# Kernel tuning notes

Hardware: AMD Instinct MI355X
Metric: run time of the kernel (lower is better)

The kernel has to match this reference:

```python
import jax, jax.numpy as jnp
import numpy as np

OBS_LEN, PRED_LEN = 20, 30
H, EMB, MLP, NOISE, HEADS = 32, 16, 64, 8, 4
N, B, G = 131072, 4096, 32  # total agents, scenes, agents per scene
NEG = -1e9


def layernorm(x, g, b, eps=1e-5):
    m = x.mean(-1, keepdims=True)
    v = ((x - m) ** 2).mean(-1, keepdims=True)
    return (x - m) / jnp.sqrt(v + eps) * g + b


def setup_inputs():
    key = jax.random.key(0)
    ks = iter(jax.random.split(key, 40))
    rn = lambda shape, s=0.1: jax.random.normal(next(ks), shape, jnp.float32) * s
    starts = np.arange(B, dtype=np.int64) * G
    return {
        "obs_traj": rn((OBS_LEN, N, 2), 1.0),
        "obs_traj_rel": rn((OBS_LEN, N, 2), 1.0),
        "start_end_seq": jnp.stack([jnp.asarray(starts), jnp.asarray(starts + G)], 1).astype(jnp.int32),
        "noise_z": rn((NOISE,), 1.0),
        "enc_emb_w": rn((EMB, 2)), "enc_emb_b": rn((EMB,)),
        "enc_wih": rn((4 * H, EMB)), "enc_whh": rn((4 * H, H)),
        "enc_bih": rn((4 * H,)), "enc_bhh": rn((4 * H,)),
        "lne_g": jnp.ones((H,), jnp.float32), "lne_b": jnp.zeros((H,), jnp.float32),
        "wq": rn((H, H)), "wk": rn((H, H)), "wv": rn((H, H)), "wo": rn((H, H)),
        "lnc_g": jnp.ones((2 * H,), jnp.float32), "lnc_b": jnp.zeros((2 * H,), jnp.float32),
        "mlp1_w": rn((MLP, 2 * H)), "mlp1_b": rn((MLP,)),
        "mlp2_w": rn((H - NOISE, MLP)), "mlp2_b": rn((H - NOISE,)),
        "dec_emb_w": rn((EMB, 2)), "dec_emb_b": rn((EMB,)),
        "dec_wih": rn((4 * H, EMB)), "dec_whh": rn((4 * H, H)),
        "dec_bih": rn((4 * H,)), "dec_bhh": rn((4 * H,)),
        "dec_out_w": rn((2, H)), "dec_out_b": rn((2,)),
    }


def _forward(obs_traj, obs_traj_rel, noise_z,
             enc_emb_w, enc_emb_b, enc_wih, enc_whh, enc_bih, enc_bhh,
             lne_g, lne_b, wq, wk, wv, wo, lnc_g, lnc_b,
             mlp1_w, mlp1_b, mlp2_w, mlp2_b,
             dec_emb_w, dec_emb_b, dec_wih, dec_whh, dec_bih, dec_bhh,
             dec_out_w, dec_out_b, se_np):
    n = obs_traj_rel.shape[1]
    # ---- Encoder: linear spatial embedding + single-layer LSTM over obs window
    emb = obs_traj_rel @ enc_emb_w.T + enc_emb_b  # (T, n, EMB)

    def enc_step(carry, x):
        h, c = carry
        gates = x @ enc_wih.T + enc_bih + h @ enc_whh.T + enc_bhh
        i, f, g, o = jnp.split(gates, 4, -1)
        c = jax.nn.sigmoid(f) * c + jax.nn.sigmoid(i) * jnp.tanh(g)
        h = jax.nn.sigmoid(o) * jnp.tanh(c)
        return (h, c), None

    z0 = jnp.zeros((n, H), emb.dtype)
    (h_enc, _), _ = jax.lax.scan(enc_step, (z0, z0), emb)
    h_enc = layernorm(h_enc, lne_g, lne_b)  # (n, H)

    # ---- Ragged per-scene self-attention, padded to max scene size
    lengths = se_np[:, 1] - se_np[:, 0]
    L = int(lengths.max())
    pos = np.arange(L)
    mask = pos[None, :] < lengths[:, None]                # (B, L) valid slots
    idx = np.where(mask, se_np[:, :1] + pos[None, :], 0)  # (B, L)
    Hp = h_enc[jnp.asarray(idx)]                          # (B, L, H)
    b = mask.shape[0]
    dh = H // HEADS

    def heads(w):
        return (Hp @ w.T).reshape(b, L, HEADS, dh).transpose(0, 2, 1, 3)

    q, k, v = heads(wq), heads(wk), heads(wv)
    scores = jnp.einsum('bhqd,bhkd->bhqk', q, k) / jnp.sqrt(jnp.float32(dh))
    scores = jnp.where(jnp.asarray(mask)[:, None, None, :], scores, NEG)
    attn = jnp.einsum('bhqk,bhkd->bhqd', jax.nn.softmax(scores, -1), v)
    attn = attn.transpose(0, 2, 1, 3).reshape(b, L, H) @ wo.T  # (B, L, H)
    flat = jnp.asarray(np.where(mask, idx, n).reshape(-1))     # invalid -> pad row n
    attn_s = jnp.zeros((n + 1, H), attn.dtype).at[flat].set(attn.reshape(-1, H))[:n]

    # ---- Decoder context MLP (LeakyReLU after every Linear, incl. last) + noise
    ctx = layernorm(jnp.concatenate([h_enc, attn_s], -1), lnc_g, lnc_b)
    x = jax.nn.leaky_relu(ctx @ mlp1_w.T + mlp1_b)
    x = jax.nn.leaky_relu(x @ mlp2_w.T + mlp2_b)  # (n, H-NOISE)
    dec_h = jnp.concatenate([x, jnp.broadcast_to(noise_z, (n, NOISE))], -1)
    dec_c = jnp.zeros_like(dec_h)

    # ---- Temporal decoder: LSTM rollout of PRED_LEN relative displacements
    def dec_step(carry, _):
        h, c, last_rel = carry
        e = last_rel @ dec_emb_w.T + dec_emb_b
        gates = e @ dec_wih.T + dec_bih + h @ dec_whh.T + dec_bhh
        i, f, g, o = jnp.split(gates, 4, -1)
        c = jax.nn.sigmoid(f) * c + jax.nn.sigmoid(i) * jnp.tanh(g)
        h = jax.nn.sigmoid(o) * jnp.tanh(c)
        rel = h @ dec_out_w.T + dec_out_b
        return (h, c, rel), rel

    _, preds = jax.lax.scan(dec_step, (dec_h, dec_c, obs_traj_rel[-1]), None, length=PRED_LEN)
    return preds  # (PRED_LEN, n, 2)


def reference(obs_traj, obs_traj_rel, start_end_seq, noise_z,
              enc_emb_w, enc_emb_b, enc_wih, enc_whh, enc_bih, enc_bhh,
              lne_g, lne_b, wq, wk, wv, wo, lnc_g, lnc_b,
              mlp1_w, mlp1_b, mlp2_w, mlp2_b,
              dec_emb_w, dec_emb_b, dec_wih, dec_whh, dec_bih, dec_bhh,
              dec_out_w, dec_out_b):
    se_np = np.asarray(start_end_seq)
    return _forward(obs_traj, obs_traj_rel, noise_z,
                    enc_emb_w, enc_emb_b, enc_wih, enc_whh, enc_bih, enc_bhh,
                    lne_g, lne_b, wq, wk, wv, wo, lnc_g, lnc_b,
                    mlp1_w, mlp1_b, mlp2_w, mlp2_b,
                    dec_emb_w, dec_emb_b, dec_wih, dec_whh, dec_bih, dec_bhh,
                    dec_out_w, dec_out_b, se_np)
```

## Files before the change

kernel.cpp:

```cpp
#include <hip/hip_runtime.h>
#include <hip/hip_bf16.h>
#include <stdint.h>

typedef unsigned short u16;
typedef unsigned int   u32;

#define NTOT 131072

typedef __bf16 bf16x8 __attribute__((ext_vector_type(8)));
typedef float  f32x4  __attribute__((ext_vector_type(4)));

typedef bf16x8 bf16x8_a __attribute__((may_alias));
typedef int4   int4_a   __attribute__((may_alias));
typedef u16    u16_a    __attribute__((may_alias));
typedef u32    u32_a    __attribute__((may_alias));
typedef float  f32_a    __attribute__((may_alias));
typedef float4 float4_a __attribute__((may_alias));
typedef float2 float2_a __attribute__((may_alias));
typedef f32x4  f32x4_a  __attribute__((may_alias));

__device__ __forceinline__ void lds_fence(){
  asm volatile("s_waitcnt lgkmcnt(0)" ::: "memory");
}

__device__ __forceinline__ float b2f(u16 u){ return __uint_as_float(((u32)u)<<16); }
__device__ __forceinline__ u16 f2b(float f){
  u32 x = __float_as_uint(f);
  return (u16)((x + 0x7fffu + ((x>>16)&1u)) >> 16);
}
__device__ __forceinline__ u16 bfb(float f){
  union { __bf16 b; u16 u; } c; c.b = (__bf16)f; return c.u;
}
__device__ __forceinline__ u32 pk2(float a, float b){
  return (u32)bfb(a) | (((u32)bfb(b))<<16);
}
__device__ __forceinline__ float ld(const u16* p, long long i, bool f32m){
  return f32m ? ((const f32_a*)p)[i] : b2f(((const u16_a*)p)[i]);
}
__device__ __forceinline__ float2 ld2(const u16* p, long long i, bool f32m){
  if (f32m) return ((const float2_a*)(const void*)p)[i];
  u32 v = ((const u32_a*)p)[i];
  float2 r; r.x = b2f((u16)(v & 0xffffu)); r.y = b2f((u16)(v >> 16)); return r;
}
__device__ __forceinline__ bool is_f32(const u16* ones){
  return ((const u32_a*)ones)[0] == 0x3F800000u;
}

__device__ __forceinline__ void lstm_cell(float i_, float f_, float g_, float o_,
                                          float& c, float& h){
  float ai = __expf(-i_);
  float ef = __expf(-f_);
  float gc = fminf(fmaxf(g_, -40.f), 40.f);
  float tg = __expf(2.f*gc);
  float t1 = (1.f+ai)*(tg+1.f);
  float num = c*t1 + (tg-1.f)*(1.f+ef);
  c = num * __builtin_amdgcn_rcpf((1.f+ef)*t1);
  float ao = __expf(-o_);
  float tc = __expf(2.f*c);
  h = (tc-1.f) * __builtin_amdgcn_rcpf((1.f+ao)*(tc+1.f));
}

__device__ __forceinline__ bf16x8 mk_frag(const u16* W, int ldW, int n, int kbase, bool f32m){
  union { bf16x8 v; u16 s[8]; } u;
  if (f32m){
    const f32_a* p = (const f32_a*)W + (size_t)n*ldW + kbase;
    float4 x0 = *reinterpret_cast<const float4_a*>(p);
    float4 x1 = *reinterpret_cast<const float4_a*>(p+4);
    u.s[0]=f2b(x0.x); u.s[1]=f2b(x0.y); u.s[2]=f2b(x0.z); u.s[3]=f2b(x0.w);
    u.s[4]=f2b(x1.x); u.s[5]=f2b(x1.y); u.s[6]=f2b(x1.z); u.s[7]=f2b(x1.w);
  } else {
    #pragma unroll
    for (int j=0;j<8;++j) u.s[j] = ((const u16_a*)W)[(size_t)n*ldW + kbase + j];
  }
  return u.v;
}
__device__ __forceinline__ void split_hilo(const float* x, bf16x8& hi, bf16x8& lo){
  union { bf16x8 v; u16 s[8]; } uh, ul;
  #pragma unroll
  for (int j=0;j<8;++j){ u16 hb=f2b(x[j]); uh.s[j]=hb; ul.s[j]=f2b(x[j]-b2f(hb)); }
  hi=uh.v; lo=ul.v;
}

__global__ void prep_kernel(const u16* __restrict__ wih, const u16* __restrict__ whh,
                            const u16* __restrict__ bih, const u16* __restrict__ bhh,
                            const u16* __restrict__ dwih, const u16* __restrict__ dwhh,
                            const u16* __restrict__ dbih, const u16* __restrict__ dbhh,
                            const u16* __restrict__ dembw, const u16* __restrict__ dembb,
                            const u16* __restrict__ doutw, const u16* __restrict__ doutb,
                            const u16* __restrict__ lng,
                            u16* __restrict__ WTe, u16* __restrict__ WTd,
                            float* __restrict__ biasd, float* __restrict__ wemo)
{
  const bool f32m = is_f32(lng);
  int tid = blockIdx.x*blockDim.x + threadIdx.x;
  int nthr = gridDim.x*blockDim.x;
  for (int idx = tid; idx < 128*96; idx += nthr){
    int rw = idx/96, k = idx - rw*96;
    float ve;
    if (k < 64){
      int kc = k & 31; int q = kc >> 3, r = kc & 7;
      int u = (r < 4) ? (q*4 + r) : (16 + q*4 + (r-4));
      ve = ld(whh, rw*32+u, f32m);
    } else {
      int kk = k - 64; int q = kk >> 3, j = kk & 7;
      if (j < 4){
        ve = ld(wih, rw*16 + q*4+j, f32m);
      } else if (q == 0 && j == 4){
        ve = ld(bih, rw, f32m) + ld(bhh, rw, f32m);
      } else if (q == 0 && j == 5){
        float bse = ld(bih, rw, f32m) + ld(bhh, rw, f32m);
        ve = bse - b2f(f2b(bse));
      } else {
        ve = 0.f;
      }
    }
    WTe[idx] = f2b(ve);
    if (k < 64){
      int kc = k & 31; int q = kc >> 3, r = kc & 7;
      int u = (r < 4) ? (q*4 + r) : (16 + q*4 + (r-4));
      float wem0 = 0.f, wem1 = 0.f;
      #pragma unroll
      for (int j=0; j<16; ++j){
        float wv = ld(dwih, rw*16+j, f32m);
        wem0 += wv*ld(dembw, j*2,   f32m);
        wem1 += wv*ld(dembw, j*2+1, f32m);
      }
      float wp = ld(dwhh, rw*32+u, f32m)
               + wem0*ld(doutw, u,    f32m)
               + wem1*ld(doutw, 32+u, f32m);
      u16 hi = f2b(wp);
      WTd[rw*64 + k] = (k < 32) ? hi : f2b(wp - b2f(hi));
    }
  }
  if (tid < 128){
    int rw = tid;
    float wem0 = 0.f, wem1 = 0.f, wdb = 0.f;
    #pragma unroll
    for (int j=0; j<16; ++j){
      float wv = ld(dwih, rw*16+j, f32m);
      wem0 += wv*ld(dembw, j*2,   f32m);
      wem1 += wv*ld(dembw, j*2+1, f32m);
      wdb  += wv*ld(dembb, j,     f32m);
    }
    float bp = ld(dbih, rw, f32m) + ld(dbhh, rw, f32m) + wdb
             + wem0*ld(doutb, 0, f32m) + wem1*ld(doutb, 1, f32m);
    biasd[rw] = bp;
    wemo[rw*2]   = wem0;
    wemo[rw*2+1] = wem1;
  }
}

__global__ __launch_bounds__(256, 1) void enc_kernel(
    const u16* __restrict__ obs_rel, const u16* __restrict__ WT,
    const u16* __restrict__ embw, const u16* __restrict__ embb,
    const u16* __restrict__ lng, const u16* __restrict__ lnb,
    float* __restrict__ hln)
{
  const bool f32m = is_f32(lng);
  const int lane = threadIdx.x & 63;
  const int wvi  = threadIdx.x >> 6;
  const int col  = lane & 15;
  const int quad = lane >> 4;
  const int base = (blockIdx.x*4 + wvi)*16;

  bf16x8 wf[8][3];
  #pragma unroll
  for (int g=0; g<8; ++g)
    #pragma unroll
    for (int c=0; c<3; ++c)
      wf[g][c] = *reinterpret_cast<const bf16x8_a*>(WT + (g*16+col)*96 + c*32 + quad*8);

  float ew0[4], ew1[4], ebv[4];
  #pragma unroll
  for (int jj=0; jj<4; ++jj){
    int j = quad*4+jj;
    ew0[jj]=ld(embw, j*2, f32m); ew1[jj]=ld(embw, j*2+1, f32m); ebv[jj]=ld(embb, j, f32m);
  }
  const u32 onespk = (quad == 0) ? 0x3F803F80u : 0u;

  union FR { bf16x8 v; u32 w[4]; };
  FR x0, x1, x2;
  x0.w[0]=x0.w[1]=x0.w[2]=x0.w[3]=0;
  x1.w[0]=x1.w[1]=x1.w[2]=x1.w[3]=0;
  x2.w[2] = onespk; x2.w[3] = 0;

  float c0[4]={0,0,0,0}, c1[4]={0,0,0,0};
  float hA[4]={0,0,0,0}, hB[4]={0,0,0,0};

  float2 rv = ld2(obs_rel, (long long)(base + col), f32m);

  #pragma unroll 1
  for (int t=0; t<20; ++t){
    float2 rnx = rv;
    if (t < 19) rnx = ld2(obs_rel, (long long)(t+1)*NTOT + base + col, f32m);
    float e0 = ew0[0]*rv.x + ew1[0]*rv.y + ebv[0];
    float e1 = ew0[1]*rv.x + ew1[1]*rv.y + ebv[1];
    float e2 = ew0[2]*rv.x + ew1[2]*rv.y + ebv[2];
    float e3 = ew0[3]*rv.x + ew1[3]*rv.y + ebv[3];
    x2.w[0] = pk2(e0, e1);
    x2.w[1] = pk2(e2, e3);

    f32x4 acc[8];
    #pragma unroll
    for (int g=0; g<8; ++g){ f32x4 zz = {0.f,0.f,0.f,0.f};
      acc[g] = __builtin_amdgcn_mfma_f32_16x16x32_bf16(wf[g][0], x0.v, zz, 0,0,0); }
    #pragma unroll
    for (int g=0; g<8; ++g)
      acc[g] = __builtin_amdgcn_mfma_f32_16x16x32_bf16(wf[g][1], x1.v, acc[g], 0,0,0);
    #pragma unroll
    for (int g=0; g<8; ++g)
      acc[g] = __builtin_amdgcn_mfma_f32_16x16x32_bf16(wf[g][2], x2.v, acc[g], 0,0,0);

    #pragma unroll
    for (int reg=0; reg<4; ++reg){
      lstm_cell(acc[0][reg], acc[2][reg], acc[4][reg], acc[6][reg], c0[reg], hA[reg]);
      lstm_cell(acc[1][reg], acc[3][reg], acc[5][reg], acc[7][reg], c1[reg], hB[reg]);
    }
    u16 a0b=bfb(hA[0]), a1b=bfb(hA[1]), a2b=bfb(hA[2]), a3b=bfb(hA[3]);
    u16 b0b=bfb(hB[0]), b1b=bfb(hB[1]), b2b=bfb(hB[2]), b3b=bfb(hB[3]);
    x0.w[0] = (u32)a0b | ((u32)a1b<<16);
    x0.w[1] = (u32)a2b | ((u32)a3b<<16);
    x0.w[2] = (u32)b0b | ((u32)b1b<<16);
    x0.w[3] = (u32)b2b | ((u32)b3b<<16);
    x1.w[0] = pk2(hA[0]-b2f(a0b), hA[1]-b2f(a1b));
    x1.w[1] = pk2(hA[2]-b2f(a2b), hA[3]-b2f(a3b));
    x1.w[2] = pk2(hB[0]-b2f(b0b), hB[1]-b2f(b1b));
    x1.w[3] = pk2(hB[2]-b2f(b2b), hB[3]-b2f(b3b));
    rv = rnx;
  }

  float sm = 0.f, sq = 0.f;
  #pragma unroll
  for (int reg=0; reg<4; ++reg){
    sm += hA[reg]+hB[reg];
    sq += hA[reg]*hA[reg]+hB[reg]*hB[reg];
  }
  sm += __shfl_xor(sm, 16, 64); sm += __shfl_xor(sm, 32, 64);
  sq += __shfl_xor(sq, 16, 64); sq += __shfl_xor(sq, 32, 64);
  float mean = sm*(1.f/32.f);
  float var  = sq*(1.f/32.f) - mean*mean;
  float rstd = rsqrtf(fmaxf(var, 0.f) + 1e-5f);
  float4 yA, yB;
  {
    float gA0=ld(lng,quad*4+0,f32m), gA1=ld(lng,quad*4+1,f32m), gA2=ld(lng,quad*4+2,f32m), gA3=ld(lng,quad*4+3,f32m);
    float bA0=ld(lnb,quad*4+0,f32m), bA1=ld(lnb,quad*4+1,f32m), bA2=ld(lnb,quad*4+2,f32m), bA3=ld(lnb,quad*4+3,f32m);
    float gB0=ld(lng,16+quad*4+0,f32m), gB1=ld(lng,16+quad*4+1,f32m), gB2=ld(lng,16+quad*4+2,f32m), gB3=ld(lng,16+quad*4+3,f32m);
    float bB0=ld(lnb,16+quad*4+0,f32m), bB1=ld(lnb,16+quad*4+1,f32m), bB2=ld(lnb,16+quad*4+2,f32m), bB3=ld(lnb,16+quad*4+3,f32m);
    yA.x=(hA[0]-mean)*rstd*gA0+bA0; yA.y=(hA[1]-mean)*rstd*gA1+bA1;
    yA.z=(hA[2]-mean)*rstd*gA2+bA2; yA.w=(hA[3]-mean)*rstd*gA3+bA3;
    yB.x=(hB[0]-mean)*rstd*gB0+bB0; yB.y=(hB[1]-mean)*rstd*gB1+bB1;
    yB.z=(hB[2]-mean)*rstd*gB2+bB2; yB.w=(hB[3]-mean)*rstd*gB3+bB3;
  }
  size_t a = (size_t)(base + col);
  *reinterpret_cast<float4_a*>(hln + a*32 + quad*4)      = yA;
  *reinterpret_cast<float4_a*>(hln + a*32 + 16 + quad*4) = yB;
}

__global__ __launch_bounds__(256, 1) void mid_kernel(
    const int* __restrict__ se, const float* __restrict__ hln,
    const u16* __restrict__ wq, const u16* __restrict__ wk,
    const u16* __restrict__ wvp, const u16* __restrict__ wo,
    const u16* __restrict__ lncg, const u16* __restrict__ lncb,
    const u16* __restrict__ m1w, const u16* __restrict__ m1b,
    const u16* __restrict__ m2w, const u16* __restrict__ m2b,
    const u16* __restrict__ noise, float* __restrict__ dech0)
{
  __shared__ float hsL[2][32][36];
  __shared__ float kL [2][32][36];
  __shared__ float vL [2][32][36];
  __shared__ float qL [2][32][36];
  __shared__ float aoL[2][32][36];
  __shared__ float cxL[4][16][68];

  const bool f32m = is_f32(lncg);
  const int lane = threadIdx.x & 63;
  const int wvi  = threadIdx.x >> 6;
  const int col  = lane & 15;
  const int quad = lane >> 4;
  const int sc_l = wvi >> 1;
  const int half = wvi & 1;
  const int a_lo = half*16;
  const int scene = blockIdx.x*2 + sc_l;

  const int s0  = se[2*scene];
  int len = se[2*scene+1] - s0;
  if (len > 32) len = 32; if (len < 0) len = 0;

  {
    int ar = a_lo + (lane>>2);
    long long g = (long long)s0 + ar;
    if (g > NTOT-1) g = NTOT-1; if (g < 0) g = 0;
    const f32_a* src = (const f32_a*)hln + g*32 + (lane&3)*8;
    float4 x0 = *reinterpret_cast<const float4_a*>(src);
    float4 x1 = *reinterpret_cast<const float4_a*>(src+4);
    float* dst = &hsL[sc_l][ar][(lane&3)*8];
    *reinterpret_cast<float4_a*>(dst)   = x0;
    *reinterpret_cast<float4_a*>(dst+4) = x1;
  }
  lds_fence();
  f32x4 z = {0.f,0.f,0.f,0.f};
  f32x4 qa0,qa1,ka0,ka1,va0,va1;
  {
    float hv[8];
    const float* r = &hsL[sc_l][a_lo+col][quad*8];
    float4 x0 = *reinterpret_cast<const float4_a*>(r);
    float4 x1 = *reinterpret_cast<const float4_a*>(r+4);
    hv[0]=x0.x; hv[1]=x0.y; hv[2]=x0.z; hv[3]=x0.w;
    hv[4]=x1.x; hv[5]=x1.y; hv[6]=x1.z; hv[7]=x1.w;
    bf16x8 ah, al; split_hilo(hv, ah, al);
    bf16x8 wqf0 = mk_frag(wq, 32, col,    quad*8, f32m);
    bf16x8 wqf1 = mk_frag(wq, 32, 16+col, quad*8, f32m);
    bf16x8 wkf0 = mk_frag(wk, 32, col,    quad*8, f32m);
    bf16x8 wkf1 = mk_frag(wk, 32, 16+col, quad*8, f32m);
    bf16x8 wvf0 = mk_frag(wvp,32, col,    quad*8, f32m);
    bf16x8 wvf1 = mk_frag(wvp,32, 16+col, quad*8, f32m);
    qa0 = __builtin_amdgcn_mfma_f32_16x16x32_bf16(ah, wqf0, z, 0,0,0);
    qa0 = __builtin_amdgcn_mfma_f32_16x16x32_bf16(al, wqf0, qa0, 0,0,0);
    qa1 = __builtin_amdgcn_mfma_f32_16x16x32_bf16(ah, wqf1, z, 0,0,0);
    qa1 = __builtin_amdgcn_mfma_f32_16x16x32_bf16(al, wqf1, qa1, 0,0,0);
    ka0 = __builtin_amdgcn_mfma_f32_16x16x32_bf16(ah, wkf0, z, 0,0,0);
    ka0 = __builtin_amdgcn_mfma_f32_16x16x32_bf16(al, wkf0, ka0, 0,0,0);
    ka1 = __builtin_amdgcn_mfma_f32_16x16x32_bf16(ah, wkf1, z, 0,0,0);
    ka1 = __builtin_amdgcn_mfma_f32_16x16x32_bf16(al, wkf1, ka1, 0,0,0);
    va0 = __builtin_amdgcn_mfma_f32_16x16x32_bf16(ah, wvf0, z, 0,0,0);
    va0 = __builtin_amdgcn_mfma_f32_16x16x32_bf16(al, wvf0, va0, 0,0,0);
    va1 = __builtin_amdgcn_mfma_f32_16x16x32_bf16(ah, wvf1, z, 0,0,0);
    va1 = __builtin_amdgcn_mfma_f32_16x16x32_bf16(al, wvf1, va1, 0,0,0);
  }
  #pragma unroll
  for (int reg=0; reg<4; ++reg){
    int ar = a_lo + quad*4 + reg;
    qL[sc_l][ar][col]    = qa0[reg];  qL[sc_l][ar][col+16] = qa1[reg];
    kL[sc_l][ar][col]    = ka0[reg];  kL[sc_l][ar][col+16] = ka1[reg];
    vL[sc_l][ar][col]    = va0[reg];  vL[sc_l][ar][col+16] = va1[reg];
  }
  __syncthreads();

  {
    int rid = half*64 + lane;
    int h  = rid >> 5, qa = rid & 31;
    const float* qrow = &qL[sc_l][qa][h*8];
    float4 q0 = *reinterpret_cast<const float4_a*>(qrow);
    float4 q1 = *reinterpret_cast<const float4_a*>(qrow+4);
    float p[32]; float mx = -3.4e38f;
    const float scale = 0.35355339059327373f;
    #pragma unroll
    for (int ka2=0; ka2<32; ++ka2){
      const float* kr = &kL[sc_l][ka2][h*8];
      float4 k0 = *reinterpret_cast<const float4_a*>(kr);
      float4 k1 = *reinterpret_cast<const float4_a*>(kr+4);
      float s = q0.x*k0.x + q0.y*k0.y + q0.z*k0.z + q0.w*k0.w
              + q1.x*k1.x + q1.y*k1.y + q1.z*k1.z + q1.w*k1.w;
      s *= scale;
      if (ka2 >= len) s = -1e9f;
      p[ka2] = s; mx = fmaxf(mx, s);
    }
    float ssum = 0.f;
    #pragma unroll
    for (int ka2=0; ka2<32; ++ka2){ float e = __expf(p[ka2]-mx); p[ka2]=e; ssum+=e; }
    float inv = __builtin_amdgcn_rcpf(ssum);
    float4 o0 = {0,0,0,0}, o1 = {0,0,0,0};
    #pragma unroll
    for (int ka2=0; ka2<32; ++ka2){
      const float* vr = &vL[sc_l][ka2][h*8];
      float4 v0 = *reinterpret_cast<const float4_a*>(vr);
      float4 v1 = *reinterpret_cast<const float4_a*>(vr+4);
      float w = p[ka2]*inv;
      o0.x += w*v0.x; o0.y += w*v0.y; o0.z += w*v0.z; o0.w += w*v0.w;
      o1.x += w*v1.x; o1.y += w*v1.y; o1.z += w*v1.z; o1.w += w*v1.w;
    }
    float* ar_ = &aoL[sc_l][qa][h*8];
    *reinterpret_cast<float4_a*>(ar_)   = o0;
    *reinterpret_cast<float4_a*>(ar_+4) = o1;
  }
  __syncthreads();

  f32x4 at0, at1;
  {
    float av[8];
    const float* r = &aoL[sc_l][a_lo+col][quad*8];
    float4 x0 = *reinterpret_cast<const float4_a*>(r);
    float4 x1 = *reinterpret_cast<const float4_a*>(r+4);
    av[0]=x0.x; av[1]=x0.y; av[2]=x0.z; av[3]=x0.w;
    av[4]=x1.x; av[5]=x1.y; av[6]=x1.z; av[7]=x1.w;
    bf16x8 aoh, aol; split_hilo(av, aoh, aol);
    bf16x8 wof0 = mk_frag(wo, 32, col,    quad*8, f32m);
    bf16x8 wof1 = mk_frag(wo, 32, 16+col, quad*8, f32m);
    at0 = __builtin_amdgcn_mfma_f32_16x16x32_bf16(aoh, wof0, z, 0,0,0);
    at0 = __builtin_amdgcn_mfma_f32_16x16x32_bf16(aol, wof0, at0, 0,0,0);
    at1 = __builtin_amdgcn_mfma_f32_16x16x32_bf16(aoh, wof1, z, 0,0,0);
    at1 = __builtin_amdgcn_mfma_f32_16x16x32_bf16(aol, wof1, at1, 0,0,0);
  }
  {
    float h0[4], h1[4], sm[4], sq[4];
    #pragma unroll
    for (int reg=0; reg<4; ++reg){
      int ar = a_lo + quad*4 + reg;
      h0[reg] = hsL[sc_l][ar][col];
      h1[reg] = hsL[sc_l][ar][col+16];
      float a0v = at0[reg], a1v = at1[reg];
      sm[reg] = h0[reg]+h1[reg]+a0v+a1v;
      sq[reg] = h0[reg]*h0[reg]+h1[reg]*h1[reg]+a0v*a0v+a1v*a1v;
    }
    #pragma unroll
    for (int m=1; m<16; m<<=1){
      #pragma unroll
      for (int reg=0; reg<4; ++reg){
        sm[reg] += __shfl_xor(sm[reg], m, 64);
        sq[reg] += __shfl_xor(sq[reg], m, 64);
      }
    }
    float g0=ld(lncg,col,f32m),    g1=ld(lncg,col+16,f32m);
    float g2=ld(lncg,col+32,f32m), g3=ld(lncg,col+48,f32m);
    float b0=ld(lncb,col,f32m),    b1=ld(lncb,col+16,f32m);
    float b2=ld(lncb,col+32,f32m), b3=ld(lncb,col+48,f32m);
    #pragma unroll
    for (int reg=0; reg<4; ++reg){
      float mean = sm[reg]*(1.f/64.f);
      float var  = sq[reg]*(1.f/64.f) - mean*mean;
      float rstd = rsqrtf(fmaxf(var,0.f) + 1e-5f);
      float* cr = &cxL[wvi][quad*4+reg][0];
      cr[col]    = (h0[reg] -mean)*rstd*g0 + b0;
      cr[col+16] = (h1[reg] -mean)*rstd*g1 + b1;
      cr[col+32] = (at0[reg]-mean)*rstd*g2 + b2;
      cr[col+48] = (at1[reg]-mean)*rstd*g3 + b3;
    }
  }
  lds_fence();
  f32x4 x1a[4];
  {
    float cv0[8], cv1[8];
    const float* r = &cxL[wvi][col][quad*8];
    float4 a0v = *reinterpret_cast<const float4_a*>(r);
    float4 a1v = *reinterpret_cast<const float4_a*>(r+4);
    const float* r2 = &cxL[wvi][col][32+quad*8];
    float4 b0v = *reinterpret_cast<const float4_a*>(r2);
    float4 b1v = *reinterpret_cast<const float4_a*>(r2+4);
    cv0[0]=a0v.x; cv0[1]=a0v.y; cv0[2]=a0v.z; cv0[3]=a0v.w;
    cv0[4]=a1v.x; cv0[5]=a1v.y; cv0[6]=a1v.z; cv0[7]=a1v.w;
    cv1[0]=b0v.x; cv1[1]=b0v.y; cv1[2]=b0v.z; cv1[3]=b0v.w;
    cv1[4]=b1v.x; cv1[5]=b1v.y; cv1[6]=b1v.z; cv1[7]=b1v.w;
    bf16x8 c0h,c0l,c1h,c1l;
    split_hilo(cv0, c0h, c0l);
    split_hilo(cv1, c1h, c1l);
    #pragma unroll
    for (int t=0; t<4; ++t){
      bf16x8 bfr0 = mk_frag(m1w, 64, t*16+col, quad*8,    f32m);
      bf16x8 bfr1 = mk_frag(m1w, 64, t*16+col, 32+quad*8, f32m);
      f32x4 acc = __builtin_amdgcn_mfma_f32_16x16x32_bf16(c0h, bfr0, z, 0,0,0);
      acc = __builtin_amdgcn_mfma_f32_16x16x32_bf16(c1h, bfr1, acc, 0,0,0);
      acc = __builtin_amdgcn_mfma_f32_16x16x32_bf16(c0l, bfr0, acc, 0,0,0);
      acc = __builtin_amdgcn_mfma_f32_16x16x32_bf16(c1l, bfr1, acc, 0,0,0);
      x1a[t] = acc;
    }
  }
  lds_fence();
  {
    #pragma unroll
    for (int t=0; t<4; ++t){
      float bv = ld(m1b, t*16+col, f32m);
      #pragma unroll
      for (int reg=0; reg<4; ++reg){
        float v = x1a[t][reg] + bv;
        v = (v > 0.f) ? v : 0.01f*v;
        cxL[wvi][quad*4+reg][t*16+col] = v;
      }
    }
  }
  lds_fence();
  {
    float yv0[8], yv1[8];
    const float* r = &cxL[wvi][col][quad*8];
    float4 a0v = *reinterpret_cast<const float4_a*>(r);
    float4 a1v = *reinterpret_cast<const float4_a*>(r+4);
    const float* r2 = &cxL[wvi][col][32+quad*8];
    float4 b0v = *reinterpret_cast<const float4_a*>(r2);
    float4 b1v = *reinterpret_cast<const float4_a*>(r2+4);
    yv0[0]=a0v.x; yv0[1]=a0v.y; yv0[2]=a0v.z; yv0[3]=a0v.w;
    yv0[4]=a1v.x; yv0[5]=a1v.y; yv0[6]=a1v.z; yv0[7]=a1v.w;
    yv1[0]=b0v.x; yv1[1]=b0v.y; yv1[2]=b0v.z; yv1[3]=b0v.w;
    yv1[4]=b1v.x; yv1[5]=b1v.y; yv1[6]=b1v.z; yv1[7]=b1v.w;
    bf16x8 y0h,y0l,y1h,y1l;
    split_hilo(yv0, y0h, y0l);
    split_hilo(yv1, y1h, y1l);
    f32x4 x2a[2];
    #pragma unroll
    for (int t=0; t<2; ++t){
      int n = t*16 + col; if (n > 23) n = 23;
      bf16x8 bfr0 = mk_frag(m2w, 64, n, quad*8,    f32m);
      bf16x8 bfr1 = mk_frag(m2w, 64, n, 32+quad*8, f32m);
      f32x4 acc = __builtin_amdgcn_mfma_f32_16x16x32_bf16(y0h, bfr0, z, 0,0,0);
      acc = __builtin_amdgcn_mfma_f32_16x16x32_bf16(y1h, bfr1, acc, 0,0,0);
      acc = __builtin_amdgcn_mfma_f32_16x16x32_bf16(y0l, bfr0, acc, 0,0,0);
      acc = __builtin_amdgcn_mfma_f32_16x16x32_bf16(y1l, bfr1, acc, 0,0,0);
      x2a[t] = acc;
    }
    float mb0 = ld(m2b, col, f32m);
    float mb1 = (col < 8) ? ld(m2b, 16+col, f32m) : 0.f;
    float nz  = (col >= 8) ? ld(noise, col-8, f32m) : 0.f;
    #pragma unroll
    for (int reg=0; reg<4; ++reg){
      int a32 = a_lo + quad*4 + reg;
      if (a32 < len){
        size_t g = ((size_t)(s0 + a32))*32;
        float v0 = x2a[0][reg] + mb0;
        v0 = (v0 > 0.f) ? v0 : 0.01f*v0;
        float v1;
        if (col < 8){
          v1 = x2a[1][reg] + mb1;
          v1 = (v1 > 0.f) ? v1 : 0.01f*v1;
        } else {
          v1 = nz;
        }
        dech0[g + col]      = v0;
        dech0[g + 16 + col] = v1;
      }
    }
  }
}

__global__ __launch_bounds__(256, 1) void dec_kernel(
    const u16* __restrict__ obs_rel, const u16* __restrict__ WT,
    const float* __restrict__ biasd, const float* __restrict__ wem,
    const u16* __restrict__ doutw, const u16* __restrict__ doutb,
    const float* __restrict__ h0in, const u16* __restrict__ lng,
    u16* __restrict__ out)
{
  const bool f32m = is_f32(lng);
  const int lane = threadIdx.x & 63;
  const int wvi  = threadIdx.x >> 6;
  const int col  = lane & 15;
  const int quad = lane >> 4;
  const int base = (blockIdx.x*4 + wvi)*16;

  bf16x8 wfA[8], wfB[8];
  #pragma unroll
  for (int g=0; g<8; ++g){
    wfA[g] = *reinterpret_cast<const bf16x8_a*>(WT + (g*16+col)*64 + quad*8);
    wfB[g] = *reinterpret_cast<const bf16x8_a*>(WT + (g*16+col)*64 + 32 + quad*8);
  }
  float w0A[4], w0B[4], w1A[4], w1B[4];
  #pragma unroll
  for (int r=0; r<4; ++r){
    w0A[r]=ld(doutw,      quad*4+r, f32m); w0B[r]=ld(doutw, 16 + quad*4+r, f32m);
    w1A[r]=ld(doutw, 32 + quad*4+r, f32m); w1B[r]=ld(doutw, 48 + quad*4+r, f32m);
  }
  float ob0=ld(doutb,0,f32m), ob1=ld(doutb,1,f32m);

  union FR { bf16x8 v; u32 w[4]; };
  FR x0, x1;
  f32x4 hA4, hB4;
  {
    const f32_a* hp = (const f32_a*)h0in + (size_t)(base+col)*32;
    hA4 = *(const f32x4_a*)(hp + quad*4);
    hB4 = *(const f32x4_a*)(hp + 16 + quad*4);
    u16 a0b=bfb(hA4[0]), a1b=bfb(hA4[1]), a2b=bfb(hA4[2]), a3b=bfb(hA4[3]);
    u16 b0b=bfb(hB4[0]), b1b=bfb(hB4[1]), b2b=bfb(hB4[2]), b3b=bfb(hB4[3]);
    x0.w[0] = (u32)a0b | ((u32)a1b<<16);
    x0.w[1] = (u32)a2b | ((u32)a3b<<16);
    x0.w[2] = (u32)b0b | ((u32)b1b<<16);
    x0.w[3] = (u32)b2b | ((u32)b3b<<16);
    x1.w[0] = pk2(hA4[0]-b2f(a0b), hA4[1]-b2f(a1b));
    x1.w[1] = pk2(hA4[2]-b2f(a2b), hA4[3]-b2f(a3b));
    x1.w[2] = pk2(hB4[0]-b2f(b0b), hB4[1]-b2f(b1b));
    x1.w[3] = pk2(hB4[2]-b2f(b2b), hB4[3]-b2f(b3b));
  }
  float2 rv = ld2(obs_rel, (long long)19*NTOT + base + col, f32m);

  f32x4 cinit[8];
  {
    float p0 = hA4[0]*w0A[0]+hA4[1]*w0A[1]+hA4[2]*w0A[2]+hA4[3]*w0A[3]
             + hB4[0]*w0B[0]+hB4[1]*w0B[1]+hB4[2]*w0B[2]+hB4[3]*w0B[3];
    float p1 = hA4[0]*w1A[0]+hA4[1]*w1A[1]+hA4[2]*w1A[2]+hA4[3]*w1A[3]
             + hB4[0]*w1B[0]+hB4[1]*w1B[1]+hB4[2]*w1B[2]+hB4[3]*w1B[3];
    p0 += __shfl_xor(p0, 16, 64); p0 += __shfl_xor(p0, 32, 64);
    p1 += __shfl_xor(p1, 16, 64); p1 += __shfl_xor(p1, 32, 64);
    float d0 = rv.x - (p0 + ob0);
    float d1 = rv.y - (p1 + ob1);
    #pragma unroll
    for (int g=0; g<8; ++g){
      #pragma unroll
      for (int reg=0; reg<4; ++reg){
        int row = g*16 + quad*4 + reg;
        float2 wm = *reinterpret_cast<const float2_a*>(wem + row*2);
        cinit[g][reg] = biasd[row] + wm.x*d0 + wm.y*d1;
      }
    }
  }

  float c0[4]={0,0,0,0}, c1[4]={0,0,0,0};
  float hA[4], hB[4];

  #pragma unroll 1
  for (int t=0; t<30; ++t){
    f32x4 acc[8];
    #pragma unroll
    for (int g=0; g<8; ++g)
      acc[g] = __builtin_amdgcn_mfma_f32_16x16x32_bf16(wfA[g], x0.v, cinit[g], 0,0,0);
    #pragma unroll
    for (int g=0; g<8; ++g)
      acc[g] = __builtin_amdgcn_mfma_f32_16x16x32_bf16(wfA[g], x1.v, acc[g], 0,0,0);
    #pragma unroll
    for (int g=0; g<8; ++g)
      acc[g] = __builtin_amdgcn_mfma_f32_16x16x32_bf16(wfB[g], x0.v, acc[g], 0,0,0);

    #pragma unroll
    for (int reg=0; reg<4; ++reg){
      lstm_cell(acc[0][reg], acc[2][reg], acc[4][reg], acc[6][reg], c0[reg], hA[reg]);
      lstm_cell(acc[1][reg], acc[3][reg], acc[5][reg], acc[7][reg], c1[reg], hB[reg]);
    }
    if (t == 0){
      #pragma unroll
      for (int g=0; g<8; ++g){
        #pragma unroll
        for (int reg=0; reg<4; ++reg)
          cinit[g][reg] = biasd[g*16 + quad*4 + reg];
      }
    }
    u16 a0b=bfb(hA[0]), a1b=bfb(hA[1]), a2b=bfb(hA[2]), a3b=bfb(hA[3]);
    u16 b0b=bfb(hB[0]), b1b=bfb(hB[1]), b2b=bfb(hB[2]), b3b=bfb(hB[3]);
    x0.w[0] = (u32)a0b | ((u32)a1b<<16);
    x0.w[1] = (u32)a2b | ((u32)a3b<<16);
    x0.w[2] = (u32)b0b | ((u32)b1b<<16);
    x0.w[3] = (u32)b2b | ((u32)b3b<<16);
    x1.w[0] = pk2(hA[0]-b2f(a0b), hA[1]-b2f(a1b));
    x1.w[1] = pk2(hA[2]-b2f(a2b), hA[3]-b2f(a3b));
    x1.w[2] = pk2(hB[0]-b2f(b0b), hB[1]-b2f(b1b));
    x1.w[3] = pk2(hB[2]-b2f(b2b), hB[3]-b2f(b3b));

    float p0 = hA[0]*w0A[0]+hA[1]*w0A[1]+hA[2]*w0A[2]+hA[3]*w0A[3]
             + hB[0]*w0B[0]+hB[1]*w0B[1]+hB[2]*w0B[2]+hB[3]*w0B[3];
    float p1 = hA[0]*w1A[0]+hA[1]*w1A[1]+hA[2]*w1A[2]+hA[3]*w1A[3]
             + hB[0]*w1B[0]+hB[1]*w1B[1]+hB[2]*w1B[2]+hB[3]*w1B[3];
    p0 += __shfl_xor(p0, 16, 64); p0 += __shfl_xor(p0, 32, 64);
    p1 += __shfl_xor(p1, 16, 64); p1 += __shfl_xor(p1, 32, 64);
    float r0o = p0 + ob0, r1o = p1 + ob1;

    if (quad == 0){
      size_t idx = (size_t)(t*NTOT + base + col);
      if (f32m){
        float2 v; v.x = r0o; v.y = r1o;
        *reinterpret_cast<float2_a*>((f32_a*)out + idx*2) = v;
      } else {
        *reinterpret_cast<u32_a*>(out + idx*2) = pk2(r0o, r1o);
      }
    }
  }
}

extern "C" void kernel_launch(void* const* d_in, const int* in_sizes, int n_in,
                              void* d_out, int out_size, void* d_ws, size_t ws_size,
                              hipStream_t stream)
{
  (void)in_sizes; (void)n_in; (void)out_size; (void)ws_size;
  const u16* obs_rel = (const u16*)d_in[1];
  const int* se      = (const int*)d_in[2];
  const u16* noise   = (const u16*)d_in[3];
  const u16* eembw = (const u16*)d_in[4];
  const u16* eembb = (const u16*)d_in[5];
  const u16* ewih  = (const u16*)d_in[6];
  const u16* ewhh  = (const u16*)d_in[7];
  const u16* ebih  = (const u16*)d_in[8];
  const u16* ebhh  = (const u16*)d_in[9];
  const u16* lneg  = (const u16*)d_in[10];
  const u16* lneb  = (const u16*)d_in[11];
  const u16* wq    = (const u16*)d_in[12];
  const u16* wk    = (const u16*)d_in[13];
  const u16* wvw   = (const u16*)d_in[14];
  const u16* wo    = (const u16*)d_in[15];
  const u16* lncg  = (const u16*)d_in[16];
  const u16* lncb  = (const u16*)d_in[17];
  const u16* m1w   = (const u16*)d_in[18];
  const u16* m1b   = (const u16*)d_in[19];
  const u16* m2w   = (const u16*)d_in[20];
  const u16* m2b   = (const u16*)d_in[21];
  const u16* dembw = (const u16*)d_in[22];
  const u16* dembb = (const u16*)d_in[23];
  const u16* dwih  = (const u16*)d_in[24];
  const u16* dwhh  = (const u16*)d_in[25];
  const u16* dbih  = (const u16*)d_in[26];
  const u16* dbhh  = (const u16*)d_in[27];
  const u16* doutw = (const u16*)d_in[28];
  const u16* doutb = (const u16*)d_in[29];

  char* ws = (char*)d_ws;
  u16*   WTe   = (u16*)(ws + 0);
  u16*   WTd   = (u16*)(ws + 24576);
  float* biasd = (float*)(ws + 40960);
  float* wem   = (float*)(ws + 41472);
  float* hln   = (float*)(ws + 65536);
  float* dech0 = (float*)(ws + 65536 + (size_t)NTOT*32*4);

  prep_kernel<<<48, 256, 0, stream>>>(ewih, ewhh, ebih, ebhh, dwih, dwhh, dbih, dbhh,
                                      dembw, dembb, doutw, doutb, lneg,
                                      WTe, WTd, biasd, wem);
  enc_kernel<<<NTOT/64, 256, 0, stream>>>(obs_rel, WTe, eembw, eembb, lneg, lneb, hln);
  mid_kernel<<<2048, 256, 0, stream>>>(se, hln, wq, wk, wvw, wo, lncg, lncb,
                                       m1w, m1b, m2w, m2b, noise, dech0);
  dec_kernel<<<NTOT/64, 256, 0, stream>>>(obs_rel, WTd, biasd, wem, doutw, doutb,
                                          dech0, lneg, (u16*)d_out);
}
```

Before: 543.0 us.

## Fold exp scaling into LSTM weights, use native exp2/packed cvt, MFMA output projection

The prep kernel now pre-scales the gate weights and biases by -log2(e), or 2*log2(e) for the g gate, so the LSTM cell can call the raw v_exp_f32 instruction with no multiplies. The cell state is carried in a scaled domain, which is why the K constant appears. Hi/lo bf16 packing uses the v_cvt_pk_bf16_f32 instruction. The decoder's per-step output projection and cross-lane shuffle reduction are replaced by three small MFMAs, and the t==0 branch is removed by peeling the first step out of the loop. The aim is to cut VALU work in the serial recurrent critical path. The risk is rounding differences from bf16 rounding of the scaled weights and from the changed clamp range.

```diff
diff --git a/kernel.cpp b/kernel.cpp
--- a/kernel.cpp
+++ b/kernel.cpp
@@ -31,8 +31,18 @@
 __device__ __forceinline__ u16 bfb(float f){
   union { __bf16 b; u16 u; } c; c.b = (__bf16)f; return c.u;
 }
-__device__ __forceinline__ u32 pk2(float a, float b){
-  return (u32)bfb(a) | (((u32)bfb(b))<<16);
+__device__ __forceinline__ u32 pkbf(float a, float b){
+  u32 r; asm("v_cvt_pk_bf16_f32 %0, %1, %2" : "=v"(r) : "v"(a), "v"(b)); return r;
+}
+__device__ __forceinline__ u32 pk2(float a, float b){ return pkbf(a, b); }
+__device__ __forceinline__ void pack_hilo2(float a, float b, u32& whi, u32& wlo){
+  whi = pkbf(a, b);
+  float l0 = a - __uint_as_float(whi << 16);
+  float l1 = b - __uint_as_float(whi & 0xffff0000u);
+  wlo = pkbf(l0, l1);
+}
+__device__ __forceinline__ float ex2(float x){
+  float r; asm("v_exp_f32 %0, %1" : "=v"(r) : "v"(x)); return r;
 }
 __device__ __forceinline__ float ld(const u16* p, long long i, bool f32m){
   return f32m ? ((const f32_a*)p)[i] : b2f(((const u16_a*)p)[i]);
@@ -46,17 +56,19 @@
   return ((const u32_a*)ones)[0] == 0x3F800000u;
 }
 
-__device__ __forceinline__ void lstm_cell(float i_, float f_, float g_, float o_,
-                                          float& c, float& h){
-  float ai = __expf(-i_);
-  float ef = __expf(-f_);
-  float gc = fminf(fmaxf(g_, -40.f), 40.f);
-  float tg = __expf(2.f*gc);
-  float t1 = (1.f+ai)*(tg+1.f);
-  float num = c*t1 + (tg-1.f)*(1.f+ef);
-  c = num * __builtin_amdgcn_rcpf((1.f+ef)*t1);
-  float ao = __expf(-o_);
-  float tc = __expf(2.f*c);
+__device__ __forceinline__ void lstm_cell2(float i2, float f2, float g2, float o2,
+                                           float& cs, float& h){
+  const float K = 2.8853900817779268f;
+  float ai = ex2(i2);
+  float ef = ex2(f2);
+  float gc = fminf(fmaxf(g2, -80.f), 80.f);
+  float tg = ex2(gc);
+  float t1  = (1.f+ai)*(tg+1.f);
+  float efp = 1.f+ef;
+  float num = cs*t1 + K*((tg-1.f)*efp);
+  cs = num * __builtin_amdgcn_rcpf(efp*t1);
+  float ao = ex2(o2);
+  float tc = ex2(cs);
   h = (tc-1.f) * __builtin_amdgcn_rcpf((1.f+ao)*(tc+1.f));
 }
 
@@ -92,23 +104,25 @@
                             float* __restrict__ biasd, float* __restrict__ wemo)
 {
   const bool f32m = is_f32(lng);
+  const float Lc = 1.4426950408889634f;
   int tid = blockIdx.x*blockDim.x + threadIdx.x;
   int nthr = gridDim.x*blockDim.x;
   for (int idx = tid; idx < 128*96; idx += nthr){
     int rw = idx/96, k = idx - rw*96;
+    const float sc = ((rw >> 5) == 2) ? 2.f*Lc : -Lc;
     float ve;
     if (k < 64){
       int kc = k & 31; int q = kc >> 3, r = kc & 7;
       int u = (r < 4) ? (q*4 + r) : (16 + q*4 + (r-4));
-      ve = ld(whh, rw*32+u, f32m);
+      ve = sc*ld(whh, rw*32+u, f32m);
     } else {
       int kk = k - 64; int q = kk >> 3, j = kk & 7;
       if (j < 4){
-        ve = ld(wih, rw*16 + q*4+j, f32m);
+        ve = sc*ld(wih, rw*16 + q*4+j, f32m);
       } else if (q == 0 && j == 4){
-        ve = ld(bih, rw, f32m) + ld(bhh, rw, f32m);
+        ve = sc*(ld(bih, rw, f32m) + ld(bhh, rw, f32m));
       } else if (q == 0 && j == 5){
-        float bse = ld(bih, rw, f32m) + ld(bhh, rw, f32m);
+        float bse = sc*(ld(bih, rw, f32m) + ld(bhh, rw, f32m));
         ve = bse - b2f(f2b(bse));
       } else {
         ve = 0.f;
@@ -125,15 +139,16 @@
         wem0 += wv*ld(dembw, j*2,   f32m);
         wem1 += wv*ld(dembw, j*2+1, f32m);
       }
-      float wp = ld(dwhh, rw*32+u, f32m)
+      float wp = sc*(ld(dwhh, rw*32+u, f32m)
                + wem0*ld(doutw, u,    f32m)
-               + wem1*ld(doutw, 32+u, f32m);
+               + wem1*ld(doutw, 32+u, f32m));
       u16 hi = f2b(wp);
       WTd[rw*64 + k] = (k < 32) ? hi : f2b(wp - b2f(hi));
     }
   }
   if (tid < 128){
     int rw = tid;
+    const float sc = ((rw >> 5) == 2) ? 2.f*Lc : -Lc;
     float wem0 = 0.f, wem1 = 0.f, wdb = 0.f;
     #pragma unroll
     for (int j=0; j<16; ++j){
@@ -144,9 +159,9 @@
     }
     float bp = ld(dbih, rw, f32m) + ld(dbhh, rw, f32m) + wdb
              + wem0*ld(doutb, 0, f32m) + wem1*ld(doutb, 1, f32m);
-    biasd[rw] = bp;
-    wemo[rw*2]   = wem0;
-    wemo[rw*2+1] = wem1;
+    biasd[rw] = sc*bp;
+    wemo[rw*2]   = sc*wem0;
+    wemo[rw*2+1] = sc*wem1;
   }
 }
 
@@ -197,8 +212,8 @@
     float e1 = ew0[1]*rv.x + ew1[1]*rv.y + ebv[1];
     float e2 = ew0[2]*rv.x + ew1[2]*rv.y + ebv[2];
     float e3 = ew0[3]*rv.x + ew1[3]*rv.y + ebv[3];
-    x2.w[0] = pk2(e0, e1);
-    x2.w[1] = pk2(e2, e3);
+    x2.w[0] = pkbf(e0, e1);
+    x2.w[1] = pkbf(e2, e3);
 
     f32x4 acc[8];
     #pragma unroll
@@ -213,19 +228,13 @@
 
     #pragma unroll
     for (int reg=0; reg<4; ++reg){
-      lstm_cell(acc[0][reg], acc[2][reg], acc[4][reg], acc[6][reg], c0[reg], hA[reg]);
-      lstm_cell(acc[1][reg], acc[3][reg], acc[5][reg], acc[7][reg], c1[reg], hB[reg]);
-    }
-    u16 a0b=bfb(hA[0]), a1b=bfb(hA[1]), a2b=bfb(hA[2]), a3b=bfb(hA[3]);
-    u16 b0b=bfb(hB[0]), b1b=bfb(hB[1]), b2b=bfb(hB[2]), b3b=bfb(hB[3]);
-    x0.w[0] = (u32)a0b | ((u32)a1b<<16);
-    x0.w[1] = (u32)a2b | ((u32)a3b<<16);
-    x0.w[2] = (u32)b0b | ((u32)b1b<<16);
-    x0.w[3] = (u32)b2b | ((u32)b3b<<16);
-    x1.w[0] = pk2(hA[0]-b2f(a0b), hA[1]-b2f(a1b));
-    x1.w[1] = pk2(hA[2]-b2f(a2b), hA[3]-b2f(a3b));
-    x1.w[2] = pk2(hB[0]-b2f(b0b), hB[1]-b2f(b1b));
-    x1.w[3] = pk2(hB[2]-b2f(b2b), hB[3]-b2f(b3b));
+      lstm_cell2(acc[0][reg], acc[2][reg], acc[4][reg], acc[6][reg], c0[reg], hA[reg]);
+      lstm_cell2(acc[1][reg], acc[3][reg], acc[5][reg], acc[7][reg], c1[reg], hB[reg]);
+    }
+    pack_hilo2(hA[0], hA[1], x0.w[0], x1.w[0]);
+    pack_hilo2(hA[2], hA[3], x0.w[1], x1.w[1]);
+    pack_hilo2(hB[0], hB[1], x0.w[2], x1.w[2]);
+    pack_hilo2(hB[2], hB[3], x0.w[3], x1.w[3]);
     rv = rnx;
   }
 
@@ -539,64 +548,67 @@
     wfA[g] = *reinterpret_cast<const bf16x8_a*>(WT + (g*16+col)*64 + quad*8);
     wfB[g] = *reinterpret_cast<const bf16x8_a*>(WT + (g*16+col)*64 + 32 + quad*8);
   }
-  float w0A[4], w0B[4], w1A[4], w1B[4];
-  #pragma unroll
-  for (int r=0; r<4; ++r){
-    w0A[r]=ld(doutw,      quad*4+r, f32m); w0B[r]=ld(doutw, 16 + quad*4+r, f32m);
-    w1A[r]=ld(doutw, 32 + quad*4+r, f32m); w1B[r]=ld(doutw, 48 + quad*4+r, f32m);
-  }
-  float ob0=ld(doutb,0,f32m), ob1=ld(doutb,1,f32m);
+  bf16x8 wouth, woutl;
+  {
+    union { bf16x8 v; u16 s[8]; } wh_, wl_;
+    #pragma unroll
+    for (int j=0; j<8; ++j){
+      int u = (j < 4) ? (quad*4 + j) : (16 + quad*4 + (j-4));
+      float w = (col < 2) ? ld(doutw, col*32 + u, f32m) : 0.f;
+      u16 hb = f2b(w);
+      wh_.s[j] = hb; wl_.s[j] = f2b(w - b2f(hb));
+    }
+    wouth = wh_.v; woutl = wl_.v;
+  }
+  f32x4 pc = {0.f,0.f,0.f,0.f};
+  if (quad == 0){ pc[0] = ld(doutb,0,f32m); pc[1] = ld(doutb,1,f32m); }
 
   union FR { bf16x8 v; u32 w[4]; };
   FR x0, x1;
-  f32x4 hA4, hB4;
   {
     const f32_a* hp = (const f32_a*)h0in + (size_t)(base+col)*32;
-    hA4 = *(const f32x4_a*)(hp + quad*4);
-    hB4 = *(const f32x4_a*)(hp + 16 + quad*4);
-    u16 a0b=bfb(hA4[0]), a1b=bfb(hA4[1]), a2b=bfb(hA4[2]), a3b=bfb(hA4[3]);
-    u16 b0b=bfb(hB4[0]), b1b=bfb(hB4[1]), b2b=bfb(hB4[2]), b3b=bfb(hB4[3]);
-    x0.w[0] = (u32)a0b | ((u32)a1b<<16);
-    x0.w[1] = (u32)a2b | ((u32)a3b<<16);
-    x0.w[2] = (u32)b0b | ((u32)b1b<<16);
-    x0.w[3] = (u32)b2b | ((u32)b3b<<16);
-    x1.w[0] = pk2(hA4[0]-b2f(a0b), hA4[1]-b2f(a1b));
-    x1.w[1] = pk2(hA4[2]-b2f(a2b), hA4[3]-b2f(a3b));
-    x1.w[2] = pk2(hB4[0]-b2f(b0b), hB4[1]-b2f(b1b));
-    x1.w[3] = pk2(hB4[2]-b2f(b2b), hB4[3]-b2f(b3b));
+    f32x4 hA4 = *(const f32x4_a*)(hp + quad*4);
+    f32x4 hB4 = *(const f32x4_a*)(hp + 16 + quad*4);
+    pack_hilo2(hA4[0], hA4[1], x0.w[0], x1.w[0]);
+    pack_hilo2(hA4[2], hA4[3], x0.w[1], x1.w[1]);
+    pack_hilo2(hB4[0], hB4[1], x0.w[2], x1.w[2]);
+    pack_hilo2(hB4[2], hB4[3], x0.w[3], x1.w[3]);
   }
   float2 rv = ld2(obs_rel, (long long)19*NTOT + base + col, f32m);
 
-  f32x4 cinit[8];
-  {
-    float p0 = hA4[0]*w0A[0]+hA4[1]*w0A[1]+hA4[2]*w0A[2]+hA4[3]*w0A[3]
-             + hB4[0]*w0B[0]+hB4[1]*w0B[1]+hB4[2]*w0B[2]+hB4[3]*w0B[3];
-    float p1 = hA4[0]*w1A[0]+hA4[1]*w1A[1]+hA4[2]*w1A[2]+hA4[3]*w1A[3]
-             + hB4[0]*w1B[0]+hB4[1]*w1B[1]+hB4[2]*w1B[2]+hB4[3]*w1B[3];
-    p0 += __shfl_xor(p0, 16, 64); p0 += __shfl_xor(p0, 32, 64);
-    p1 += __shfl_xor(p1, 16, 64); p1 += __shfl_xor(p1, 32, 64);
-    float d0 = rv.x - (p0 + ob0);
-    float d1 = rv.y - (p1 + ob1);
+  f32x4 biasr[8];
+  #pragma unroll
+  for (int g=0; g<8; ++g)
+    biasr[g] = *(const f32x4_a*)(biasd + g*16 + quad*4);
+
+  f32x4 cf[8];
+  {
+    f32x4 a2 = __builtin_amdgcn_mfma_f32_16x16x32_bf16(wouth, x0.v, pc, 0,0,0);
+    a2 = __builtin_amdgcn_mfma_f32_16x16x32_bf16(wouth, x1.v, a2, 0,0,0);
+    a2 = __builtin_amdgcn_mfma_f32_16x16x32_bf16(woutl, x0.v, a2, 0,0,0);
+    float p0b = __shfl(a2[0], col, 64);
+    float p1b = __shfl(a2[1], col, 64);
+    float d0 = rv.x - p0b;
+    float d1 = rv.y - p1b;
     #pragma unroll
     for (int g=0; g<8; ++g){
-      #pragma unroll
-      for (int reg=0; reg<4; ++reg){
-        int row = g*16 + quad*4 + reg;
-        float2 wm = *reinterpret_cast<const float2_a*>(wem + row*2);
-        cinit[g][reg] = biasd[row] + wm.x*d0 + wm.y*d1;
-      }
+      const float4_a* wp = (const float4_a*)(wem + (size_t)(g*16 + quad*4)*2);
+      float4 wa = wp[0], wb = wp[1];
+      cf[g][0] = biasr[g][0] + wa.x*d0 + wa.y*d1;
+      cf[g][1] = biasr[g][1] + wa.z*d0 + wa.w*d1;
+      cf[g][2] = biasr[g][2] + wb.x*d0 + wb.y*d1;
+      cf[g][3] = biasr[g][3] + wb.z*d0 + wb.w*d1;
     }
   }
 
   float c0[4]={0,0,0,0}, c1[4]={0,0,0,0};
   float hA[4], hB[4];
 
-  #pragma unroll 1
-  for (int t=0; t<30; ++t){
+  auto dstep = [&](const f32x4 (&cin)[8], int t){
     f32x4 acc[8];
     #pragma unroll
     for (int g=0; g<8; ++g)
-      acc[g] = __builtin_amdgcn_mfma_f32_16x16x32_bf16(wfA[g], x0.v, cinit[g], 0,0,0);
+      acc[g] = __builtin_amdgcn_mfma_f32_16x16x32_bf16(wfA[g], x0.v, cin[g], 0,0,0);
     #pragma unroll
     for (int g=0; g<8; ++g)
       acc[g] = __builtin_amdgcn_mfma_f32_16x16x32_bf16(wfA[g], x1.v, acc[g], 0,0,0);
@@ -606,46 +618,32 @@
 
     #pragma unroll
     for (int reg=0; reg<4; ++reg){
-      lstm_cell(acc[0][reg], acc[2][reg], acc[4][reg], acc[6][reg], c0[reg], hA[reg]);
-      lstm_cell(acc[1][reg], acc[3][reg], acc[5][reg], acc[7][reg], c1[reg], hB[reg]);
-    }
-    if (t == 0){
-      #pragma unroll
-      for (int g=0; g<8; ++g){
-        #pragma unroll
-        for (int reg=0; reg<4; ++reg)
-          cinit[g][reg] = biasd[g*16 + quad*4 + reg];
-      }
-    }
-    u16 a0b=bfb(hA[0]), a1b=bfb(hA[1]), a2b=bfb(hA[2]), a3b=bfb(hA[3]);
-    u16 b0b=bfb(hB[0]), b1b=bfb(hB[1]), b2b=bfb(hB[2]), b3b=bfb(hB[3]);
-    x0.w[0] = (u32)a0b | ((u32)a1b<<16);
-    x0.w[1] = (u32)a2b | ((u32)a3b<<16);
-    x0.w[2] = (u32)b0b | ((u32)b1b<<16);
-    x0.w[3] = (u32)b2b | ((u32)b3b<<16);
-    x1.w[0] = pk2(hA[0]-b2f(a0b), hA[1]-b2f(a1b));
-    x1.w[1] = pk2(hA[2]-b2f(a2b), hA[3]-b2f(a3b));
-    x1.w[2] = pk2(hB[0]-b2f(b0b), hB[1]-b2f(b1b));
-    x1.w[3] = pk2(hB[2]-b2f(b2b), hB[3]-b2f(b3b));
-
-    float p0 = hA[0]*w0A[0]+hA[1]*w0A[1]+hA[2]*w0A[2]+hA[3]*w0A[3]
-             + hB[0]*w0B[0]+hB[1]*w0B[1]+hB[2]*w0B[2]+hB[3]*w0B[3];
-    float p1 = hA[0]*w1A[0]+hA[1]*w1A[1]+hA[2]*w1A[2]+hA[3]*w1A[3]
-             + hB[0]*w1B[0]+hB[1]*w1B[1]+hB[2]*w1B[2]+hB[3]*w1B[3];
-    p0 += __shfl_xor(p0, 16, 64); p0 += __shfl_xor(p0, 32, 64);
-    p1 += __shfl_xor(p1, 16, 64); p1 += __shfl_xor(p1, 32, 64);
-    float r0o = p0 + ob0, r1o = p1 + ob1;
+      lstm_cell2(acc[0][reg], acc[2][reg], acc[4][reg], acc[6][reg], c0[reg], hA[reg]);
+      lstm_cell2(acc[1][reg], acc[3][reg], acc[5][reg], acc[7][reg], c1[reg], hB[reg]);
+    }
+    pack_hilo2(hA[0], hA[1], x0.w[0], x1.w[0]);
+    pack_hilo2(hA[2], hA[3], x0.w[1], x1.w[1]);
+    pack_hilo2(hB[0], hB[1], x0.w[2], x1.w[2]);
+    pack_hilo2(hB[2], hB[3], x0.w[3], x1.w[3]);
+
+    f32x4 a2 = __builtin_amdgcn_mfma_f32_16x16x32_bf16(wouth, x0.v, pc, 0,0,0);
+    a2 = __builtin_amdgcn_mfma_f32_16x16x32_bf16(wouth, x1.v, a2, 0,0,0);
+    a2 = __builtin_amdgcn_mfma_f32_16x16x32_bf16(woutl, x0.v, a2, 0,0,0);
 
     if (quad == 0){
       size_t idx = (size_t)(t*NTOT + base + col);
       if (f32m){
-        float2 v; v.x = r0o; v.y = r1o;
+        float2 v; v.x = a2[0]; v.y = a2[1];
         *reinterpret_cast<float2_a*>((f32_a*)out + idx*2) = v;
       } else {
-        *reinterpret_cast<u32_a*>(out + idx*2) = pk2(r0o, r1o);
+        *reinterpret_cast<u32_a*>(out + idx*2) = pkbf(a2[0], a2[1]);
       }
     }
-  }
+  };
+
+  dstep(cf, 0);
+  #pragma unroll 1
+  for (int t=1; t<30; ++t) dstep(biasr, t);
 }
 
 extern "C" void kernel_launch(void* const* d_in, const int* in_sizes, int n_in,
```

New measurement: 478.3 us (median of 2 runs). 11.9% less time.
